# Optimization experiments

Measured on AMD Instinct MI355X. Metric: run time of the kernel, lower is better.

The kernel has to match this reference:

```python
import jax, jax.numpy as jnp
import numpy as np


def setup_inputs() -> dict:
    key = jax.random.key(0)
    ks = jax.random.split(key, 4)
    B, Tq, Tv, D = 8, 256, 512, 256  # decoder_dim = D = 256
    query = jax.random.normal(ks[0], (B, Tq, D), dtype=jnp.float32)
    value = jax.random.normal(ks[1], (B, Tv, D), dtype=jnp.float32)
    W1 = jax.random.normal(ks[2], (D, D), dtype=jnp.float32) * (1.0 / np.sqrt(D))
    b1 = jnp.zeros((D,), dtype=jnp.float32)
    W2 = jax.random.normal(ks[3], (D, D), dtype=jnp.float32) * (1.0 / np.sqrt(D))
    b2 = jnp.zeros((D,), dtype=jnp.float32)
    return {"query": query, "value": value, "W1": W1, "b1": b1, "W2": W2, "b2": b2}


def reference(query, value, W1, b1, W2, b2):
    # Dense projections: [B,Tq,D], [B,Tv,D]
    q = jnp.einsum('bqd,de->bqe', query, W1) + b1
    v = jnp.einsum('bvd,de->bve', value, W2) + b2
    # Additive (Bahdanau) score: broadcast tanh then reduce over feature dim
    # score: [B,Tq,Tv]  (intermediate [B,Tq,Tv,D] is the fusion target)
    score = jnp.tanh(q[:, :, None, :] + v[:, None, :, :]).sum(axis=-1)
    alignment = jax.nn.softmax(score, axis=-1)  # [B,Tq,Tv]
    context = jnp.einsum('bqv,bvd->bqd', alignment, value)  # [B,Tq,D]
    context = jnp.concatenate([context, query], axis=-1)  # [B,Tq,2D]
    alignment_t = jnp.transpose(alignment, (0, 2, 1))  # [B,Tv,Tq]
    return context, alignment_t
```

## Files before the change

kernel.cpp:

```cpp
#include <hip/hip_runtime.h>

#define B_  8
#define TQ  256
#define TV  512
#define DD  256
#define ALGS 520

__device__ __forceinline__ float fast_exp2(float x) {
#if __has_builtin(__builtin_amdgcn_exp2f)
  return __builtin_amdgcn_exp2f(x);
#else
  return __exp2f(x);
#endif
}
__device__ __forceinline__ float fast_rcp(float x) {
#if __has_builtin(__builtin_amdgcn_rcpf)
  return __builtin_amdgcn_rcpf(x);
#else
  return 1.0f / x;
#endif
}

__global__ __launch_bounds__(256) void proj_fused(
    const float* __restrict__ query, const float* __restrict__ value,
    const float* __restrict__ W1, const float* __restrict__ b1,
    const float* __restrict__ W2, const float* __restrict__ b2,
    float* __restrict__ qp, float* __restrict__ vp, float scale) {
  __shared__ float As[2][32][64];
  __shared__ float Bs[2][32][64];
  const int t  = threadIdx.x;
  const int rt = blockIdx.x;
  const int bn = blockIdx.y << 6;

  const float* A; const float* W; const float* bias; float* out; int row0;
  if (rt < 32) { row0 = rt << 6;        A = query; W = W1; bias = b1; out = qp; }
  else         { row0 = (rt - 32) << 6; A = value; W = W2; bias = b2; out = vp; }

  const int tx = t & 15, ty = t >> 4;
  const int aar = t >> 3, aac = (t & 7) << 2;
  const int bbr = t >> 4, bbc = (t & 15) << 2;

  float4 ra[2], rb[2];
#pragma unroll
  for (int it = 0; it < 2; ++it) {
    ra[it] = *(const float4*)(A + (size_t)(row0 + (it << 5) + aar) * DD + aac);
    rb[it] = *(const float4*)(W + (size_t)((it << 4) + bbr) * DD + bn + bbc);
  }
#pragma unroll
  for (int it = 0; it < 2; ++it) {
    const int m = (it << 5) + aar;
#pragma unroll
    for (int c = 0; c < 4; ++c) {
      const int k = aac + c;
      As[0][k][m ^ (((k >> 2) & 7) << 2)] = (&ra[it].x)[c];
    }
    *(float4*)&Bs[0][(it << 4) + bbr][bbc] = rb[it];
  }
  __syncthreads();

  float acc[4][4] = {{0.f,0.f,0.f,0.f},{0.f,0.f,0.f,0.f},
                     {0.f,0.f,0.f,0.f},{0.f,0.f,0.f,0.f}};
  int p = 0;

  for (int k0 = 0; k0 < 256; k0 += 32) {
    const bool more = (k0 + 32) < 256;
    if (more) {
#pragma unroll
      for (int it = 0; it < 2; ++it) {
        ra[it] = *(const float4*)(A + (size_t)(row0 + (it << 5) + aar) * DD + k0 + 32 + aac);
        rb[it] = *(const float4*)(W + (size_t)(k0 + 32 + (it << 4) + bbr) * DD + bn + bbc);
      }
    }
#pragma unroll
    for (int k = 0; k < 32; ++k) {
      float4 aq = *(const float4*)&As[p][k][(ty << 2) ^ (((k >> 2) & 7) << 2)];
      float4 bq = *(const float4*)&Bs[p][k][tx << 2];
      acc[0][0] = fmaf(aq.x, bq.x, acc[0][0]); acc[0][1] = fmaf(aq.x, bq.y, acc[0][1]);
      acc[0][2] = fmaf(aq.x, bq.z, acc[0][2]); acc[0][3] = fmaf(aq.x, bq.w, acc[0][3]);
      acc[1][0] = fmaf(aq.y, bq.x, acc[1][0]); acc[1][1] = fmaf(aq.y, bq.y, acc[1][1]);
      acc[1][2] = fmaf(aq.y, bq.z, acc[1][2]); acc[1][3] = fmaf(aq.y, bq.w, acc[1][3]);
      acc[2][0] = fmaf(aq.z, bq.x, acc[2][0]); acc[2][1] = fmaf(aq.z, bq.y, acc[2][1]);
      acc[2][2] = fmaf(aq.z, bq.z, acc[2][2]); acc[2][3] = fmaf(aq.z, bq.w, acc[2][3]);
      acc[3][0] = fmaf(aq.w, bq.x, acc[3][0]); acc[3][1] = fmaf(aq.w, bq.y, acc[3][1]);
      acc[3][2] = fmaf(aq.w, bq.z, acc[3][2]); acc[3][3] = fmaf(aq.w, bq.w, acc[3][3]);
    }
    if (more) {
      const int q = p ^ 1;
#pragma unroll
      for (int it = 0; it < 2; ++it) {
        const int m = (it << 5) + aar;
#pragma unroll
        for (int c = 0; c < 4; ++c) {
          const int k = aac + c;
          As[q][k][m ^ (((k >> 2) & 7) << 2)] = (&ra[it].x)[c];
        }
        *(float4*)&Bs[q][(it << 4) + bbr][bbc] = rb[it];
      }
      __syncthreads();
      p = q;
    }
  }

  float4 bvv = *(const float4*)&bias[bn + (tx << 2)];
#pragma unroll
  for (int r = 0; r < 4; ++r) {
    float4 o;
    o.x = fast_exp2(scale * (acc[r][0] + bvv.x));
    o.y = fast_exp2(scale * (acc[r][1] + bvv.y));
    o.z = fast_exp2(scale * (acc[r][2] + bvv.z));
    o.w = fast_exp2(scale * (acc[r][3] + bvv.w));
    *(float4*)(out + (size_t)(row0 + (ty << 2) + r) * DD + bn + (tx << 2)) = o;
  }
}

__global__ __launch_bounds__(512, 4) void attn_kernel(
    const float* __restrict__ qp, const float* __restrict__ vp,
    const float* __restrict__ value, const float* __restrict__ query,
    float* __restrict__ out1, float* __restrict__ out2) {
  __shared__ float qs[4 * 256];
  __shared__ float alg[4 * ALGS];

  const int t    = threadIdx.x;
  const int lane = t & 63;
  const int wv   = t >> 6;
  const int jj   = lane >> 2;
  const int dq   = lane & 3;
  const int bb   = blockIdx.x & 7;
  const int i0   = (blockIdx.x >> 3) << 2;

  const float* vpb = vp + (size_t)bb * TV * DD;
  const float* qb  = qp + (size_t)(bb * TQ + i0) * DD;

  if (t < 256) {
    const int qi = t >> 6, qc = (t & 63) << 2;
    *(float4*)&qs[qi * 256 + qc] = *(const float4*)(qb + (size_t)qi * DD + qc);
  }
  __syncthreads();

  const int jb = (wv << 4) + jj;
  const float* vr0 = vpb + (size_t)jb * DD + (dq << 2);
  const float* vr1 = vr0 + 128 * DD;
  const float* vr2 = vr0 + 256 * DD;
  const float* vr3 = vr0 + 384 * DD;
  const float* qlane = qs + (dq << 2);

  float acc[4][4] = {{0.f,0.f,0.f,0.f},{0.f,0.f,0.f,0.f},
                     {0.f,0.f,0.f,0.f},{0.f,0.f,0.f,0.f}};

  float4 vn0 = *(const float4*)(vr0);
  float4 vn1 = *(const float4*)(vr1);
  float4 vn2 = *(const float4*)(vr2);
  float4 vn3 = *(const float4*)(vr3);
  float4 qn0 = *(const float4*)(qlane + 0 * 256);
  float4 qn1 = *(const float4*)(qlane + 1 * 256);
  float4 qn2 = *(const float4*)(qlane + 2 * 256);
  float4 qn3 = *(const float4*)(qlane + 3 * 256);

#pragma unroll 1
  for (int k = 0; k < 16; ++k) {
    float4 vc0 = vn0, vc1 = vn1, vc2 = vn2, vc3 = vn3;
    float4 q0 = qn0, q1 = qn1, q2 = qn2, q3 = qn3;
    if (k < 15) {
      const int dn = (k + 1) << 4;
      vn0 = *(const float4*)(vr0 + dn);
      vn1 = *(const float4*)(vr1 + dn);
      vn2 = *(const float4*)(vr2 + dn);
      vn3 = *(const float4*)(vr3 + dn);
      qn0 = *(const float4*)(qlane + 0 * 256 + dn);
      qn1 = *(const float4*)(qlane + 1 * 256 + dn);
      qn2 = *(const float4*)(qlane + 2 * 256 + dn);
      qn3 = *(const float4*)(qlane + 3 * 256 + dn);
    }
#pragma unroll
    for (int jg = 0; jg < 4; ++jg) {
      const float4 v4 = (jg == 0) ? vc0 : (jg == 1) ? vc1 : (jg == 2) ? vc2 : vc3;
#pragma unroll
      for (int i = 0; i < 4; ++i) {
        const float4 q4 = (i == 0) ? q0 : (i == 1) ? q1 : (i == 2) ? q2 : q3;
        float a = q4.x * v4.x, b = q4.y * v4.y;
        float c = q4.z * v4.z, d = q4.w * v4.w;
        float sab = a + b,  scd = c + d;
        float Q1 = fmaf(a, b, sab + 1.f);
        float Q2 = fmaf(c, d, scd + 1.f);
        float N  = fmaf(scd + 2.f, Q1, (sab + 2.f) * Q2);
        acc[i][jg] = fmaf(N, fast_rcp(Q1 * Q2), acc[i][jg]);
      }
    }
  }

#pragma unroll
  for (int i = 0; i < 4; ++i)
#pragma unroll
    for (int jg = 0; jg < 4; ++jg) {
      acc[i][jg] += __shfl_xor(acc[i][jg], 1, 64);
      acc[i][jg] += __shfl_xor(acc[i][jg], 2, 64);
    }
#pragma unroll
  for (int jg = 0; jg < 4; ++jg) {
    float x = (dq == 0) ? acc[0][jg] : (dq == 1) ? acc[1][jg]
            : (dq == 2) ? acc[2][jg] : acc[3][jg];
    alg[dq * ALGS + (jg << 7) + jb] = x;
  }
  __syncthreads();

  if (wv < 4) {
    float s[8];
#pragma unroll
    for (int c = 0; c < 8; ++c) s[c] = alg[wv * ALGS + (c << 6) + lane];
    float mn = s[0];
#pragma unroll
    for (int c = 1; c < 8; ++c) mn = fminf(mn, s[c]);
#pragma unroll
    for (int m = 1; m < 64; m <<= 1) mn = fminf(mn, __shfl_xor(mn, m, 64));

    const float CC = 2.8853900817779268f;
    float p[8];
    float sum = 0.f;
#pragma unroll
    for (int c = 0; c < 8; ++c) { p[c] = fast_exp2(CC * (mn - s[c])); sum += p[c]; }
#pragma unroll
    for (int m = 1; m < 64; m <<= 1) sum += __shfl_xor(sum, m, 64);
    const float inv = fast_rcp(sum);
#pragma unroll
    for (int c = 0; c < 8; ++c) alg[wv * ALGS + (c << 6) + lane] = p[c] * inv;
  }
  __syncthreads();

  {
    const int j = t;
    float4 av = make_float4(alg[j], alg[ALGS + j], alg[2 * ALGS + j], alg[3 * ALGS + j]);
    *(float4*)(out2 + (size_t)(bb * TV + j) * TQ + i0) = av;
  }

  const int f  = t & 255;
  const int rp = t >> 8;
  float c0 = 0.f, c1 = 0.f;
  const float* vb = value + (size_t)bb * TV * DD;
  const float* a0p = &alg[(2 * rp + 0) * ALGS];
  const float* a1p = &alg[(2 * rp + 1) * ALGS];
#pragma unroll 4
  for (int j = 0; j < TV; j += 4) {
    float v0 = vb[(size_t)(j + 0) * DD + f];
    float v1 = vb[(size_t)(j + 1) * DD + f];
    float v2 = vb[(size_t)(j + 2) * DD + f];
    float v3 = vb[(size_t)(j + 3) * DD + f];
    float4 a0 = *(const float4*)&a0p[j];
    float4 a1 = *(const float4*)&a1p[j];
    c0 += a0.x * v0 + a0.y * v1 + a0.z * v2 + a0.w * v3;
    c1 += a1.x * v0 + a1.y * v1 + a1.z * v2 + a1.w * v3;
  }

  const int r0_ = (rp << 1), r1_ = r0_ + 1;
  const float* qg = query + (size_t)(bb * TQ + i0) * DD;
  float* o = out1 + (size_t)(bb * TQ + i0) * (2 * DD);
  o[r0_ * 512 + f] = c0; o[r0_ * 512 + 256 + f] = qg[r0_ * DD + f];
  o[r1_ * 512 + f] = c1; o[r1_ * 512 + 256 + f] = qg[r1_ * DD + f];
}

extern "C" void kernel_launch(void* const* d_in, const int* in_sizes, int n_in,
                              void* d_out, int out_size, void* d_ws, size_t ws_size,
                              hipStream_t stream) {
  const float* query = (const float*)d_in[0];
  const float* value = (const float*)d_in[1];
  const float* W1    = (const float*)d_in[2];
  const float* b1    = (const float*)d_in[3];
  const float* W2    = (const float*)d_in[4];
  const float* b2    = (const float*)d_in[5];

  float* out1 = (float*)d_out;
  float* out2 = out1 + (size_t)B_ * TQ * 2 * DD;

  float* qp = (float*)d_ws;
  float* vp = qp + (size_t)B_ * TQ * DD;

  const float SC = 2.8853900817779268f;

  proj_fused<<<dim3(96, 4), 256, 0, stream>>>(query, value, W1, b1, W2, b2, qp, vp, SC);
  attn_kernel<<<dim3(B_ * (TQ / 4)), 512, 0, stream>>>(qp, vp, value, query, out1, out2);
}
```

Measured before the change: 139.6 us.

## Double attention block to 1024 threads and split context reduction over key halves

Measured after the change: 159.6 us. 1.14x slower.

```diff
diff --git a/kernel.cpp b/kernel.cpp
--- a/kernel.cpp
+++ b/kernel.cpp
@@ -113,12 +113,13 @@
   }
 }
 
-__global__ __launch_bounds__(512, 4) void attn_kernel(
+__global__ __launch_bounds__(1024, 8) void attn_kernel(
     const float* __restrict__ qp, const float* __restrict__ vp,
     const float* __restrict__ value, const float* __restrict__ query,
     float* __restrict__ out1, float* __restrict__ out2) {
   __shared__ float qs[4 * 256];
   __shared__ float alg[4 * ALGS];
+  __shared__ float part[2048];
 
   const int t    = threadIdx.x;
   const int lane = t & 63;
@@ -139,18 +140,13 @@
 
   const int jb = (wv << 4) + jj;
   const float* vr0 = vpb + (size_t)jb * DD + (dq << 2);
-  const float* vr1 = vr0 + 128 * DD;
-  const float* vr2 = vr0 + 256 * DD;
-  const float* vr3 = vr0 + 384 * DD;
+  const float* vr1 = vr0 + 256 * DD;
   const float* qlane = qs + (dq << 2);
 
-  float acc[4][4] = {{0.f,0.f,0.f,0.f},{0.f,0.f,0.f,0.f},
-                     {0.f,0.f,0.f,0.f},{0.f,0.f,0.f,0.f}};
+  float acc[4][2] = {{0.f,0.f},{0.f,0.f},{0.f,0.f},{0.f,0.f}};
 
   float4 vn0 = *(const float4*)(vr0);
   float4 vn1 = *(const float4*)(vr1);
-  float4 vn2 = *(const float4*)(vr2);
-  float4 vn3 = *(const float4*)(vr3);
   float4 qn0 = *(const float4*)(qlane + 0 * 256);
   float4 qn1 = *(const float4*)(qlane + 1 * 256);
   float4 qn2 = *(const float4*)(qlane + 2 * 256);
@@ -158,22 +154,20 @@
 
 #pragma unroll 1
   for (int k = 0; k < 16; ++k) {
-    float4 vc0 = vn0, vc1 = vn1, vc2 = vn2, vc3 = vn3;
+    float4 vc0 = vn0, vc1 = vn1;
     float4 q0 = qn0, q1 = qn1, q2 = qn2, q3 = qn3;
     if (k < 15) {
       const int dn = (k + 1) << 4;
       vn0 = *(const float4*)(vr0 + dn);
       vn1 = *(const float4*)(vr1 + dn);
-      vn2 = *(const float4*)(vr2 + dn);
-      vn3 = *(const float4*)(vr3 + dn);
       qn0 = *(const float4*)(qlane + 0 * 256 + dn);
       qn1 = *(const float4*)(qlane + 1 * 256 + dn);
       qn2 = *(const float4*)(qlane + 2 * 256 + dn);
       qn3 = *(const float4*)(qlane + 3 * 256 + dn);
     }
 #pragma unroll
-    for (int jg = 0; jg < 4; ++jg) {
-      const float4 v4 = (jg == 0) ? vc0 : (jg == 1) ? vc1 : (jg == 2) ? vc2 : vc3;
+    for (int jg = 0; jg < 2; ++jg) {
+      const float4 v4 = (jg == 0) ? vc0 : vc1;
 #pragma unroll
       for (int i = 0; i < 4; ++i) {
         const float4 q4 = (i == 0) ? q0 : (i == 1) ? q1 : (i == 2) ? q2 : q3;
@@ -191,15 +185,15 @@
 #pragma unroll
   for (int i = 0; i < 4; ++i)
 #pragma unroll
-    for (int jg = 0; jg < 4; ++jg) {
+    for (int jg = 0; jg < 2; ++jg) {
       acc[i][jg] += __shfl_xor(acc[i][jg], 1, 64);
       acc[i][jg] += __shfl_xor(acc[i][jg], 2, 64);
     }
 #pragma unroll
-  for (int jg = 0; jg < 4; ++jg) {
+  for (int jg = 0; jg < 2; ++jg) {
     float x = (dq == 0) ? acc[0][jg] : (dq == 1) ? acc[1][jg]
             : (dq == 2) ? acc[2][jg] : acc[3][jg];
-    alg[dq * ALGS + (jg << 7) + jb] = x;
+    alg[dq * ALGS + (jg << 8) + jb] = x;
   }
   __syncthreads();
 
@@ -226,20 +220,22 @@
   }
   __syncthreads();
 
-  {
+  if (t < 512) {
     const int j = t;
     float4 av = make_float4(alg[j], alg[ALGS + j], alg[2 * ALGS + j], alg[3 * ALGS + j]);
     *(float4*)(out2 + (size_t)(bb * TV + j) * TQ + i0) = av;
   }
 
   const int f  = t & 255;
-  const int rp = t >> 8;
+  const int rp = (t >> 8) & 1;
+  const int jh = t >> 9;
   float c0 = 0.f, c1 = 0.f;
   const float* vb = value + (size_t)bb * TV * DD;
   const float* a0p = &alg[(2 * rp + 0) * ALGS];
   const float* a1p = &alg[(2 * rp + 1) * ALGS];
+  const int jbeg = jh << 8;
 #pragma unroll 4
-  for (int j = 0; j < TV; j += 4) {
+  for (int j = jbeg; j < jbeg + 256; j += 4) {
     float v0 = vb[(size_t)(j + 0) * DD + f];
     float v1 = vb[(size_t)(j + 1) * DD + f];
     float v2 = vb[(size_t)(j + 2) * DD + f];
@@ -249,12 +245,20 @@
     c0 += a0.x * v0 + a0.y * v1 + a0.z * v2 + a0.w * v3;
     c1 += a1.x * v0 + a1.y * v1 + a1.z * v2 + a1.w * v3;
   }
-
-  const int r0_ = (rp << 1), r1_ = r0_ + 1;
-  const float* qg = query + (size_t)(bb * TQ + i0) * DD;
-  float* o = out1 + (size_t)(bb * TQ + i0) * (2 * DD);
-  o[r0_ * 512 + f] = c0; o[r0_ * 512 + 256 + f] = qg[r0_ * DD + f];
-  o[r1_ * 512 + f] = c1; o[r1_ * 512 + 256 + f] = qg[r1_ * DD + f];
+  part[(jh << 10) + (rp << 9) + f]       = c0;
+  part[(jh << 10) + (rp << 9) + 256 + f] = c1;
+  __syncthreads();
+
+  {
+    const int row = t >> 8;
+    const int rpp = row >> 1, rw = row & 1;
+    const float cfull = part[(rpp << 9) + (rw << 8) + f]
+                      + part[1024 + (rpp << 9) + (rw << 8) + f];
+    const float* qg = query + (size_t)(bb * TQ + i0) * DD;
+    float* o = out1 + (size_t)(bb * TQ + i0) * (2 * DD);
+    o[row * 512 + f]       = cfull;
+    o[row * 512 + 256 + f] = qg[row * DD + f];
+  }
 }
 
 extern "C" void kernel_launch(void* const* d_in, const int* in_sizes, int n_in,
@@ -276,5 +280,5 @@
   const float SC = 2.8853900817779268f;
 
   proj_fused<<<dim3(96, 4), 256, 0, stream>>>(query, value, W1, b1, W2, b2, qp, vp, SC);
-  attn_kernel<<<dim3(B_ * (TQ / 4)), 512, 0, stream>>>(qp, vp, value, query, out1, out2);
-}
+  attn_kernel<<<dim3(B_ * (TQ / 4)), 1024, 0, stream>>>(qp, vp, value, query, out1, out2);
+}
```
